# Performance work log

Hardware: AMD Instinct MI355X
Metric: run time of the kernel (lower is better)

## Reference

```python
import jax, jax.numpy as jnp
import numpy as np

N_NODES = 59392        # batch_size * node_each_graph = 512 * 116
N_EDGES = 1187840      # avg degree 20

def _graph_conv(h, src, dst, W, b, out_norm, in_norm):
    # DGL GraphConv, norm='both': act((D_in^-1/2 A D_out^-1/2 h) W + b)
    h = h * out_norm[:, None]
    m = jax.ops.segment_sum(h[src], dst, num_segments=N_NODES)  # sparse aggregation
    m = m * in_norm[:, None]
    return jax.nn.relu(m @ W + b)

def setup_inputs() -> dict:
    key = jax.random.key(0)
    ks = jax.random.split(key, 8)
    feat = jax.random.normal(ks[0], (N_NODES, 116), dtype=jnp.float32)
    src = jax.random.randint(ks[1], (N_EDGES,), 0, N_NODES)
    dst = jax.random.randint(ks[2], (N_EDGES,), 0, N_NODES)
    W1 = jax.random.normal(ks[3], (116, 64), dtype=jnp.float32) * 0.05
    b1 = jnp.zeros((64,), dtype=jnp.float32)
    W2 = jax.random.normal(ks[4], (64, 64), dtype=jnp.float32) * 0.05
    b2 = jnp.zeros((64,), dtype=jnp.float32)
    Wc = jax.random.normal(ks[5], (116 * 64, 2), dtype=jnp.float32) * 0.05
    bc = jnp.zeros((2,), dtype=jnp.float32)
    return {"feat": feat, "src": src, "dst": dst, "batch_size": 512,
            "W1": W1, "b1": b1, "W2": W2, "b2": b2, "Wc": Wc, "bc": bc}

def reference(feat, src, dst, batch_size, W1, b1, W2, b2, Wc, bc):
    ones = jnp.ones((N_EDGES,), dtype=jnp.float32)
    out_deg = jax.ops.segment_sum(ones, src, num_segments=N_NODES)
    in_deg = jax.ops.segment_sum(ones, dst, num_segments=N_NODES)
    out_norm = jax.lax.rsqrt(jnp.maximum(out_deg, 1.0))
    in_norm = jax.lax.rsqrt(jnp.maximum(in_deg, 1.0))
    h = _graph_conv(feat, src, dst, W1, b1, out_norm, in_norm)
    # dropout is identity in eval mode
    h = _graph_conv(h, src, dst, W2, b2, out_norm, in_norm)
    h = h.reshape(batch_size, -1)  # (B, node_each_graph * hid)
    return h @ Wc + bc
```

## Files before the change

### kernel.cpp

```cpp
#include <hip/hip_runtime.h>

#define N_NODES 59392
#define N_EDGES 1187840
#define F_IN 116
#define F_HID 64
#define BATCH 512
#define NPG 116
#define CCAP 64
#define NSLD 160
#define EPSD (N_EDGES / NSLD)
#define NSLS 64
#define EPSS (N_EDGES / NSLS)
#define NR 4
#define NPR4 (N_NODES / NR)
#define GPB 4
#define NPB (NPG / GPB)
#define SCAN_BLK (N_NODES / 256)
#define GEMM_BLK 640

typedef __attribute__((ext_vector_type(8))) short short8;
typedef __attribute__((ext_vector_type(4))) float float4v;

__device__ __forceinline__ float u2f(unsigned u) {
    union { unsigned u; float f; } x; x.u = u; return x.f;
}
__device__ __forceinline__ float bf2f(unsigned short h) {
    union { unsigned u; float f; } x; x.u = (unsigned)h << 16; return x.f;
}
__device__ __forceinline__ unsigned short f2bf(float f) {
    union { float f; unsigned u; } x; x.f = f;
    unsigned r = x.u + 0x7FFF + ((x.u >> 16) & 1);
    return (unsigned short)(r >> 16);
}

__global__ __launch_bounds__(256) void hist_kernel(const int* __restrict__ src,
                                                   const int* __restrict__ dst,
                                                   unsigned short* __restrict__ cnt2,
                                                   unsigned short* __restrict__ cnt2s) {
    __shared__ unsigned bins[NPR4 / 2];
    int tid = threadIdx.x;
    int b = blockIdx.x;
    const int* __restrict__ idx;
    unsigned short* outp;
    int slice, range, nedge;
    if (b < NSLD * NR) {
        slice = b >> 2; range = b & 3; idx = dst; outp = cnt2; nedge = EPSD;
    } else {
        int bb = b - NSLD * NR;
        slice = bb >> 2; range = bb & 3; idx = src; outp = cnt2s; nedge = EPSS;
    }
    int r0 = range * NPR4;
    long ebase = (long)slice * nedge;
    for (int k = tid; k < NPR4 / 2; k += 256) bins[k] = 0;
    __syncthreads();
    for (int k = tid; k < nedge; k += 256) {
        int v = idx[ebase + k] - r0;
        if ((unsigned)v < NPR4) atomicAdd(&bins[v >> 1], 1u << ((v & 1) * 16));
    }
    __syncthreads();
    unsigned* op = (unsigned*)(outp + (size_t)slice * N_NODES + r0);
    for (int k = tid; k < NPR4 / 2; k += 256) op[k] = bins[k];
}

__global__ __launch_bounds__(256) void scan_gemm1_kernel(unsigned short* __restrict__ cnt2,
                                                         const unsigned short* __restrict__ cnt2s,
                                                         float* __restrict__ onorm,
                                                         float* __restrict__ inorm,
                                                         int* __restrict__ ncnt,
                                                         const float* __restrict__ feat,
                                                         const float* __restrict__ W1,
                                                         unsigned short* __restrict__ A1h) {
    if (blockIdx.x < SCAN_BLK) {
        int d = blockIdx.x * 256 + threadIdx.x;
        int run = 0;
        #pragma unroll 1
        for (int i = 0; i < NSLD; i += 8) {
            int c[8];
            #pragma unroll
            for (int j = 0; j < 8; ++j) c[j] = cnt2[(size_t)(i + j) * N_NODES + d];
            #pragma unroll
            for (int j = 0; j < 8; ++j) {
                cnt2[(size_t)(i + j) * N_NODES + d] = (unsigned short)run;
                run += c[j];
            }
        }
        int o = 0;
        #pragma unroll 1
        for (int i = 0; i < NSLS; i += 8) {
            int c[8];
            #pragma unroll
            for (int j = 0; j < 8; ++j) c[j] = cnt2s[(size_t)(i + j) * N_NODES + d];
            #pragma unroll
            for (int j = 0; j < 8; ++j) o += c[j];
        }
        onorm[d] = rsqrtf(fmaxf((float)o, 1.0f));
        inorm[d] = rsqrtf(fmaxf((float)run, 1.0f));
        ncnt[d] = run < CCAP ? run : CCAP;
        if (d == 0) onorm[N_NODES] = 0.f;
        return;
    }
    int lane = threadIdx.x & 63;
    int c16 = lane & 15, quad = lane >> 4;
    short8 Bhi[4][4], Blo[4][4];
    #pragma unroll
    for (int kiter = 0; kiter < 4; ++kiter) {
        #pragma unroll
        for (int t = 0; t < 4; ++t) {
            #pragma unroll
            for (int j = 0; j < 8; ++j) {
                int k = kiter * 32 + quad * 8 + j;
                float w = (k < F_IN) ? W1[k * F_HID + t * 16 + c16] : 0.f;
                unsigned short hi = f2bf(w);
                unsigned short lo = f2bf(w - bf2f(hi));
                Bhi[kiter][t][j] = (short)hi;
                Blo[kiter][t][j] = (short)lo;
            }
        }
    }
    int bid = blockIdx.x - SCAN_BLK;
    int wid = (bid * 256 + threadIdx.x) >> 6;
    int nwaves = (GEMM_BLK * 256) >> 6;
    const int ntiles = N_NODES / 16;
    for (int tile = wid; tile < ntiles; tile += nwaves) {
        int base = tile * 16;
        int row = base + c16;
        const float* fp = feat + (size_t)row * F_IN;
        float4v acc[4] = {{0.f,0.f,0.f,0.f},{0.f,0.f,0.f,0.f},{0.f,0.f,0.f,0.f},{0.f,0.f,0.f,0.f}};
        #pragma unroll
        for (int kiter = 0; kiter < 4; ++kiter) {
            int koff = kiter * 32 + quad * 8;
            float f[8];
            if (koff + 8 <= F_IN) {
                float4 x = *(const float4*)(fp + koff);
                float4 y = *(const float4*)(fp + koff + 4);
                f[0]=x.x; f[1]=x.y; f[2]=x.z; f[3]=x.w;
                f[4]=y.x; f[5]=y.y; f[6]=y.z; f[7]=y.w;
            } else {
                #pragma unroll
                for (int j = 0; j < 8; ++j) f[j] = (koff + j < F_IN) ? fp[koff + j] : 0.f;
            }
            short8 ah, al;
            #pragma unroll
            for (int j = 0; j < 8; ++j) {
                float v = f[j];
                unsigned short hi = f2bf(v);
                ah[j] = (short)hi;
                al[j] = (short)f2bf(v - bf2f(hi));
            }
            #pragma unroll
            for (int t = 0; t < 4; ++t) {
                acc[t] = __builtin_amdgcn_mfma_f32_16x16x32_bf16(ah, Bhi[kiter][t], acc[t], 0, 0, 0);
                acc[t] = __builtin_amdgcn_mfma_f32_16x16x32_bf16(al, Bhi[kiter][t], acc[t], 0, 0, 0);
                acc[t] = __builtin_amdgcn_mfma_f32_16x16x32_bf16(ah, Blo[kiter][t], acc[t], 0, 0, 0);
            }
        }
        #pragma unroll
        for (int t = 0; t < 4; ++t) {
            #pragma unroll
            for (int r = 0; r < 4; ++r) {
                int node = base + quad * 4 + r;
                A1h[(size_t)node * F_HID + t * 16 + c16] = f2bf(acc[t][r]);
            }
        }
    }
}

__global__ __launch_bounds__(256) void place_kernel(const int* __restrict__ src,
                                                    const int* __restrict__ dst,
                                                    const unsigned short* __restrict__ cnt2,
                                                    unsigned short* __restrict__ ebuf) {
    __shared__ unsigned cur[NPR4 / 2];
    int tid = threadIdx.x;
    int slice = blockIdx.x >> 2;
    int r0 = (blockIdx.x & 3) * NPR4;
    long ebase = (long)slice * EPSD;
    const unsigned* pp = (const unsigned*)(cnt2 + (size_t)slice * N_NODES + r0);
    for (int k = tid; k < NPR4 / 2; k += 256) cur[k] = pp[k];
    __syncthreads();
    #pragma unroll 1
    for (int t = 0; t < 7; ++t) {
        int k = t * 1024 + tid;
        int d0 = dst[ebase + k],        s0 = src[ebase + k];
        int d1 = dst[ebase + k + 256],  s1 = src[ebase + k + 256];
        int d2 = dst[ebase + k + 512],  s2 = src[ebase + k + 512];
        int d3 = dst[ebase + k + 768],  s3 = src[ebase + k + 768];
        #define PLACE1(dd, ss)                                                    \
            { int dr = (dd) - r0;                                                 \
              if ((unsigned)dr < NPR4) {                                          \
                  int sh = (dr & 1) * 16;                                         \
                  unsigned old = atomicAdd(&cur[dr >> 1], 1u << sh);              \
                  unsigned pos = (old >> sh) & 0xFFFFu;                           \
                  if (pos < CCAP) ebuf[(size_t)(dd) * CCAP + pos] = (unsigned short)(ss); } }
        PLACE1(d0, s0) PLACE1(d1, s1) PLACE1(d2, s2) PLACE1(d3, s3)
    }
    {
        int k = 7168 + tid;
        int d0 = dst[ebase + k], s0 = src[ebase + k];
        PLACE1(d0, s0)
        #undef PLACE1
    }
}

template<bool ON>
__device__ __forceinline__ void gather2n(const unsigned* __restrict__ base,
                                         const unsigned short* __restrict__ ebuf,
                                         const float* __restrict__ onorm,
                                         int va, int vb, int na, int nb,
                                         int c16, int g4, int sh16,
                                         float& a0, float& a1, float& a2, float& a3,
                                         float& b0, float& b1, float& b2, float& b3) {
    const unsigned long long* ea = (const unsigned long long*)(ebuf + (size_t)va * CCAP);
    const unsigned long long* eb = (const unsigned long long*)(ebuf + (size_t)vb * CCAP);
    unsigned long long cha[8], chb[8];
    #pragma unroll
    for (int t = 0; t < 8; ++t) cha[t] = __builtin_nontemporal_load(&ea[t]);
    #pragma unroll
    for (int t = 0; t < 8; ++t) chb[t] = __builtin_nontemporal_load(&eb[t]);
    int ida[8], idb[8];
    #pragma unroll
    for (int t = 0; t < 8; ++t) {
        ida[t] = (t * 4 + g4 < na) ? (int)((cha[t] >> sh16) & 0xFFFFu) : N_NODES;
        idb[t] = (t * 4 + g4 < nb) ? (int)((chb[t] >> sh16) & 0xFFFFu) : N_NODES;
    }
    unsigned long long rwa[8], rwb[8];
    #pragma unroll
    for (int t = 0; t < 8; ++t) rwa[t] = *(const unsigned long long*)(base + ida[t] * 32 + c16 * 2);
    #pragma unroll
    for (int t = 0; t < 8; ++t) rwb[t] = *(const unsigned long long*)(base + idb[t] * 32 + c16 * 2);
    float oa[8], ob[8];
    if constexpr (ON) {
        #pragma unroll
        for (int t = 0; t < 8; ++t) { oa[t] = onorm[ida[t]]; ob[t] = onorm[idb[t]]; }
    }
    #pragma unroll
    for (int t = 0; t < 8; ++t) {
        unsigned lo = (unsigned)rwa[t], hi = (unsigned)(rwa[t] >> 32);
        float s = ON ? oa[t] : 1.f;
        a0 += s * u2f(lo << 16); a1 += s * u2f(lo & 0xFFFF0000u);
        a2 += s * u2f(hi << 16); a3 += s * u2f(hi & 0xFFFF0000u);
    }
    #pragma unroll
    for (int t = 0; t < 8; ++t) {
        unsigned lo = (unsigned)rwb[t], hi = (unsigned)(rwb[t] >> 32);
        float s = ON ? ob[t] : 1.f;
        b0 += s * u2f(lo << 16); b1 += s * u2f(lo & 0xFFFF0000u);
        b2 += s * u2f(hi << 16); b3 += s * u2f(hi & 0xFFFF0000u);
    }
    int nqa = (na + 3) >> 2;
    #pragma unroll 1
    for (int t = 8; t < nqa; ++t) {
        unsigned long long c = __builtin_nontemporal_load(&ea[t]);
        int e = t * 4 + g4;
        int ix = (e < na) ? (int)((c >> sh16) & 0xFFFFu) : N_NODES;
        unsigned long long w = *(const unsigned long long*)(base + ix * 32 + c16 * 2);
        unsigned lo = (unsigned)w, hi = (unsigned)(w >> 32);
        float s = 1.f;
        if constexpr (ON) s = onorm[ix];
        a0 += s * u2f(lo << 16); a1 += s * u2f(lo & 0xFFFF0000u);
        a2 += s * u2f(hi << 16); a3 += s * u2f(hi & 0xFFFF0000u);
    }
    int nqb = (nb + 3) >> 2;
    #pragma unroll 1
    for (int t = 8; t < nqb; ++t) {
        unsigned long long c = __builtin_nontemporal_load(&eb[t]);
        int e = t * 4 + g4;
        int ix = (e < nb) ? (int)((c >> sh16) & 0xFFFFu) : N_NODES;
        unsigned long long w = *(const unsigned long long*)(base + ix * 32 + c16 * 2);
        unsigned lo = (unsigned)w, hi = (unsigned)(w >> 32);
        float s = 1.f;
        if constexpr (ON) s = onorm[ix];
        b0 += s * u2f(lo << 16); b1 += s * u2f(lo & 0xFFFF0000u);
        b2 += s * u2f(hi << 16); b3 += s * u2f(hi & 0xFFFF0000u);
    }
    a0 += __shfl_xor(a0, 16); a1 += __shfl_xor(a1, 16);
    a2 += __shfl_xor(a2, 16); a3 += __shfl_xor(a3, 16);
    a0 += __shfl_xor(a0, 32); a1 += __shfl_xor(a1, 32);
    a2 += __shfl_xor(a2, 32); a3 += __shfl_xor(a3, 32);
    b0 += __shfl_xor(b0, 16); b1 += __shfl_xor(b1, 16);
    b2 += __shfl_xor(b2, 16); b3 += __shfl_xor(b3, 16);
    b0 += __shfl_xor(b0, 32); b1 += __shfl_xor(b1, 32);
    b2 += __shfl_xor(b2, 32); b3 += __shfl_xor(b3, 32);
}

__global__ __launch_bounds__(256) void gather1_kernel(const int* __restrict__ ncnt,
                                                      const unsigned short* __restrict__ ebuf,
                                                      const unsigned short* __restrict__ A1h,
                                                      const float* __restrict__ onorm,
                                                      const float* __restrict__ inorm,
                                                      const float* __restrict__ b1,
                                                      unsigned short* __restrict__ H1h,
                                                      float* __restrict__ out) {
    if (blockIdx.x == 0) {
        int t = threadIdx.x;
        for (int k = t; k < BATCH * 2; k += 256) out[k] = 0.f;
        if (t < 16) ((unsigned long long*)(H1h + (size_t)N_NODES * F_HID))[t] = 0ull;
    }
    int lane = threadIdx.x & 63;
    int wu = __builtin_amdgcn_readfirstlane(threadIdx.x >> 6);
    int c16 = lane & 15, g4 = lane >> 4, sh16 = g4 * 16;
    int va = blockIdx.x * 8 + wu * 2;
    int vb = va + 1;
    int na = ncnt[va], nb = ncnt[vb];
    const unsigned* base = (const unsigned*)A1h;
    float4 b1q = ((const float4*)b1)[c16];
    float a0 = 0.f, a1 = 0.f, a2 = 0.f, a3 = 0.f;
    float b0 = 0.f, b1v = 0.f, b2v = 0.f, b3 = 0.f;
    gather2n<true>(base, ebuf, onorm, va, vb, na, nb, c16, g4, sh16,
                   a0, a1, a2, a3, b0, b1v, b2v, b3);
    float ina = inorm[va], ona = onorm[va];
    float inb = inorm[vb], onb = onorm[vb];
    float ha0 = fmaxf(ina * a0 + b1q.x, 0.f) * ona;
    float ha1 = fmaxf(ina * a1 + b1q.y, 0.f) * ona;
    float ha2 = fmaxf(ina * a2 + b1q.z, 0.f) * ona;
    float ha3 = fmaxf(ina * a3 + b1q.w, 0.f) * ona;
    float hb0 = fmaxf(inb * b0 + b1q.x, 0.f) * onb;
    float hb1 = fmaxf(inb * b1v + b1q.y, 0.f) * onb;
    float hb2 = fmaxf(inb * b2v + b1q.z, 0.f) * onb;
    float hb3 = fmaxf(inb * b3 + b1q.w, 0.f) * onb;
    if (g4 == 0) {
        unsigned lo = (unsigned)f2bf(ha0) | ((unsigned)f2bf(ha1) << 16);
        unsigned hi = (unsigned)f2bf(ha2) | ((unsigned)f2bf(ha3) << 16);
        ((unsigned long long*)H1h)[(size_t)va * 16 + c16] = ((unsigned long long)hi << 32) | lo;
        lo = (unsigned)f2bf(hb0) | ((unsigned)f2bf(hb1) << 16);
        hi = (unsigned)f2bf(hb2) | ((unsigned)f2bf(hb3) << 16);
        ((unsigned long long*)H1h)[(size_t)vb * 16 + c16] = ((unsigned long long)hi << 32) | lo;
    }
}

__global__ __launch_bounds__(256) void readout_kernel(const int* __restrict__ ncnt,
                                                      const unsigned short* __restrict__ ebuf,
                                                      const unsigned short* __restrict__ H1h,
                                                      const float* __restrict__ inorm,
                                                      const float* __restrict__ b2,
                                                      const float* __restrict__ W2,
                                                      const float* __restrict__ Wc,
                                                      const float* __restrict__ bc,
                                                      float* __restrict__ out) {
    __shared__ float Gs[NPB][F_HID];
    __shared__ float ls[8];
    int g = blockIdx.x >> 2, part = blockIdx.x & 3;
    int nbase = g * NPG + part * NPB;
    int lane = threadIdx.x & 63;
    int wu = __builtin_amdgcn_readfirstlane(threadIdx.x >> 6);
    int c16 = lane & 15, g4 = lane >> 4, sh16 = g4 * 16;
    const unsigned* base = (const unsigned*)H1h;
    for (int nl = wu * 2; nl + 1 < NPB; nl += 8) {
        int va = nbase + nl, vb = va + 1;
        int na = ncnt[va], nb = ncnt[vb];
        float a0 = 0.f, a1 = 0.f, a2 = 0.f, a3 = 0.f;
        float b0 = 0.f, b1 = 0.f, b2v = 0.f, b3 = 0.f;
        gather2n<false>(base, ebuf, (const float*)nullptr, va, vb, na, nb, c16, g4, sh16,
                        a0, a1, a2, a3, b0, b1, b2v, b3);
        if (g4 == 0) {
            float4 m4; m4.x = a0; m4.y = a1; m4.z = a2; m4.w = a3;
            *(float4*)&Gs[nl][c16 * 4] = m4;
            m4.x = b0; m4.y = b1; m4.z = b2v; m4.w = b3;
            *(float4*)&Gs[nl + 1][c16 * 4] = m4;
        }
    }
    if (wu == 2) {
        int v = nbase + 28;
        int n = ncnt[v];
        float a0 = 0.f, a1 = 0.f, a2 = 0.f, a3 = 0.f;
        float d0 = 0.f, d1 = 0.f, d2 = 0.f, d3 = 0.f;
        gather2n<false>(base, ebuf, (const float*)nullptr, v, v, n, 0, c16, g4, sh16,
                        a0, a1, a2, a3, d0, d1, d2, d3);
        if (g4 == 0) {
            float4 m4; m4.x = a0; m4.y = a1; m4.z = a2; m4.w = a3;
            *(float4*)&Gs[28][c16 * 4] = m4;
        }
    }
    __syncthreads();
    float w2[F_HID];
    #pragma unroll
    for (int k = 0; k < F_HID; ++k) w2[k] = W2[k * F_HID + lane];
    float b2l = b2[lane];
    float s0 = 0.f, s1 = 0.f;
    for (int nl = wu; nl < NPB; nl += 4) {
        int v = nbase + nl;
        float acc = 0.f;
        #pragma unroll
        for (int k = 0; k < F_HID; k += 4) {
            float4 gk = *(const float4*)&Gs[nl][k];
            acc += gk.x * w2[k] + gk.y * w2[k + 1] + gk.z * w2[k + 2] + gk.w * w2[k + 3];
        }
        float h = fmaxf(inorm[v] * acc + b2l, 0.f);
        float2 w = ((const float2*)Wc)[(part * NPB + nl) * F_HID + lane];
        s0 += h * w.x;
        s1 += h * w.y;
    }
    #pragma unroll
    for (int off = 32; off > 0; off >>= 1) {
        s0 += __shfl_down(s0, off);
        s1 += __shfl_down(s1, off);
    }
    if (lane == 0) { ls[wu * 2] = s0; ls[wu * 2 + 1] = s1; }
    __syncthreads();
    if (threadIdx.x < 2) {
        float t = 0.f;
        #pragma unroll
        for (int w = 0; w < 4; ++w) t += ls[w * 2 + threadIdx.x];
        if (part == 0) t += bc[threadIdx.x];
        atomicAdd(&out[g * 2 + threadIdx.x], t);
    }
}

extern "C" void kernel_launch(void* const* d_in, const int* in_sizes, int n_in,
                              void* d_out, int out_size, void* d_ws, size_t ws_size,
                              hipStream_t stream) {
    const float* feat = (const float*)d_in[0];
    const int*   src  = (const int*)d_in[1];
    const int*   dst  = (const int*)d_in[2];
    const float* W1 = (const float*)d_in[4];
    const float* b1 = (const float*)d_in[5];
    const float* W2 = (const float*)d_in[6];
    const float* b2 = (const float*)d_in[7];
    const float* Wc = (const float*)d_in[8];
    const float* bc = (const float*)d_in[9];
    float* out = (float*)d_out;

    unsigned short* cnt2  = (unsigned short*)d_ws;
    unsigned short* cnt2s = cnt2 + (size_t)NSLD * N_NODES;
    float* onorm = (float*)(cnt2s + (size_t)NSLS * N_NODES);
    float* inorm = onorm + N_NODES + 1;
    int* ncnt    = (int*)(inorm + N_NODES);
    unsigned short* ebuf = (unsigned short*)(ncnt + N_NODES);
    unsigned short* A1h  = ebuf + (size_t)N_NODES * CCAP;
    unsigned short* H1h  = cnt2;

    hist_kernel<<<NSLD * NR + NSLS * NR, 256, 0, stream>>>(src, dst, cnt2, cnt2s);
    scan_gemm1_kernel<<<SCAN_BLK + GEMM_BLK, 256, 0, stream>>>(cnt2, cnt2s, onorm, inorm,
                                                               ncnt, feat, W1, A1h);
    place_kernel<<<NSLD * NR, 256, 0, stream>>>(src, dst, cnt2, ebuf);
    gather1_kernel<<<N_NODES / 8, 256, 0, stream>>>(ncnt, ebuf, A1h, onorm, inorm, b1, H1h, out);
    readout_kernel<<<BATCH * GPB, 256, 0, stream>>>(ncnt, ebuf, H1h, inorm, b2, W2, Wc, bc, out);
}
```

Before: 225.0 us.

## Replace sliced histogram/scan/place with global atomic edge bucketing fused into GEMM1

Drops the per-slice LDS histograms, prefix scan and separate placement pass. Edges are now bucketed by destination with global atomics on degree counters, in blocks that run alongside the first-layer MFMA GEMM blocks. A small zero kernel runs first. Degree norms are recomputed on the fly with rsqrt instead of being stored, which removes several kernels and the large count arrays. The cost is heavy global atomic contention, and neighbour order within each bucket is now nondeterministic, so float summation order can vary between runs.

```diff
diff --git a/kernel.cpp b/kernel.cpp
--- a/kernel.cpp
+++ b/kernel.cpp
@@ -7,19 +7,15 @@
 #define BATCH 512
 #define NPG 116
 #define CCAP 64
-#define NSLD 160
-#define EPSD (N_EDGES / NSLD)
-#define NSLS 64
-#define EPSS (N_EDGES / NSLS)
-#define NR 4
-#define NPR4 (N_NODES / NR)
 #define GPB 4
 #define NPB (NPG / GPB)
-#define SCAN_BLK (N_NODES / 256)
 #define GEMM_BLK 640
+#define BUILD_BLK 512
+#define ZERO_BLK 64
 
 typedef __attribute__((ext_vector_type(8))) short short8;
 typedef __attribute__((ext_vector_type(4))) float float4v;
+typedef __attribute__((ext_vector_type(4))) int int4v;
 
 __device__ __forceinline__ float u2f(unsigned u) {
     union { unsigned u; float f; } x; x.u = u; return x.f;
@@ -33,70 +29,54 @@
     return (unsigned short)(r >> 16);
 }
 
-__global__ __launch_bounds__(256) void hist_kernel(const int* __restrict__ src,
-                                                   const int* __restrict__ dst,
-                                                   unsigned short* __restrict__ cnt2,
-                                                   unsigned short* __restrict__ cnt2s) {
-    __shared__ unsigned bins[NPR4 / 2];
-    int tid = threadIdx.x;
-    int b = blockIdx.x;
-    const int* __restrict__ idx;
-    unsigned short* outp;
-    int slice, range, nedge;
-    if (b < NSLD * NR) {
-        slice = b >> 2; range = b & 3; idx = dst; outp = cnt2; nedge = EPSD;
-    } else {
-        int bb = b - NSLD * NR;
-        slice = bb >> 2; range = bb & 3; idx = src; outp = cnt2s; nedge = EPSS;
-    }
-    int r0 = range * NPR4;
-    long ebase = (long)slice * nedge;
-    for (int k = tid; k < NPR4 / 2; k += 256) bins[k] = 0;
-    __syncthreads();
-    for (int k = tid; k < nedge; k += 256) {
-        int v = idx[ebase + k] - r0;
-        if ((unsigned)v < NPR4) atomicAdd(&bins[v >> 1], 1u << ((v & 1) * 16));
-    }
-    __syncthreads();
-    unsigned* op = (unsigned*)(outp + (size_t)slice * N_NODES + r0);
-    for (int k = tid; k < NPR4 / 2; k += 256) op[k] = bins[k];
-}
-
-__global__ __launch_bounds__(256) void scan_gemm1_kernel(unsigned short* __restrict__ cnt2,
-                                                         const unsigned short* __restrict__ cnt2s,
-                                                         float* __restrict__ onorm,
-                                                         float* __restrict__ inorm,
-                                                         int* __restrict__ ncnt,
-                                                         const float* __restrict__ feat,
-                                                         const float* __restrict__ W1,
-                                                         unsigned short* __restrict__ A1h) {
-    if (blockIdx.x < SCAN_BLK) {
-        int d = blockIdx.x * 256 + threadIdx.x;
-        int run = 0;
+__global__ __launch_bounds__(256) void zero_kernel(unsigned* __restrict__ odeg,
+                                                   unsigned* __restrict__ icnt,
+                                                   unsigned short* __restrict__ A1h,
+                                                   unsigned short* __restrict__ H1h,
+                                                   float* __restrict__ out) {
+    int gid = blockIdx.x * 256 + threadIdx.x;
+    for (int k = gid; k < N_NODES + 1; k += ZERO_BLK * 256) {
+        odeg[k] = 0u;
+        icnt[k] = 0u;
+    }
+    if (blockIdx.x == 0) {
+        if (threadIdx.x < 16) {
+            ((unsigned long long*)(A1h + (size_t)N_NODES * F_HID))[threadIdx.x] = 0ull;
+            ((unsigned long long*)(H1h + (size_t)N_NODES * F_HID))[threadIdx.x] = 0ull;
+        }
+        for (int k = threadIdx.x; k < BATCH * 2; k += 256) out[k] = 0.f;
+    }
+}
+
+__global__ __launch_bounds__(256) void build_gemm1_kernel(const int* __restrict__ src,
+                                                          const int* __restrict__ dst,
+                                                          unsigned* __restrict__ odeg,
+                                                          unsigned* __restrict__ icnt,
+                                                          unsigned short* __restrict__ ebuf,
+                                                          const float* __restrict__ feat,
+                                                          const float* __restrict__ W1,
+                                                          unsigned short* __restrict__ A1h) {
+    if (blockIdx.x >= GEMM_BLK) {
+        int gid = (blockIdx.x - GEMM_BLK) * 256 + threadIdx.x;
+        const int4v* s4 = (const int4v*)src;
+        const int4v* d4 = (const int4v*)dst;
         #pragma unroll 1
-        for (int i = 0; i < NSLD; i += 8) {
-            int c[8];
-            #pragma unroll
-            for (int j = 0; j < 8; ++j) c[j] = cnt2[(size_t)(i + j) * N_NODES + d];
-            #pragma unroll
-            for (int j = 0; j < 8; ++j) {
-                cnt2[(size_t)(i + j) * N_NODES + d] = (unsigned short)run;
-                run += c[j];
-            }
-        }
-        int o = 0;
-        #pragma unroll 1
-        for (int i = 0; i < NSLS; i += 8) {
-            int c[8];
-            #pragma unroll
-            for (int j = 0; j < 8; ++j) c[j] = cnt2s[(size_t)(i + j) * N_NODES + d];
-            #pragma unroll
-            for (int j = 0; j < 8; ++j) o += c[j];
-        }
-        onorm[d] = rsqrtf(fmaxf((float)o, 1.0f));
-        inorm[d] = rsqrtf(fmaxf((float)run, 1.0f));
-        ncnt[d] = run < CCAP ? run : CCAP;
-        if (d == 0) onorm[N_NODES] = 0.f;
+        for (int k = gid; k < N_EDGES / 4; k += BUILD_BLK * 256) {
+            int4v s = __builtin_nontemporal_load(&s4[k]);
+            int4v d = __builtin_nontemporal_load(&d4[k]);
+            atomicAdd(&odeg[s.x], 1u);
+            atomicAdd(&odeg[s.y], 1u);
+            atomicAdd(&odeg[s.z], 1u);
+            atomicAdd(&odeg[s.w], 1u);
+            unsigned p0 = atomicAdd(&icnt[d.x], 1u);
+            unsigned p1 = atomicAdd(&icnt[d.y], 1u);
+            unsigned p2 = atomicAdd(&icnt[d.z], 1u);
+            unsigned p3 = atomicAdd(&icnt[d.w], 1u);
+            if (p0 < CCAP) ebuf[(size_t)d.x * CCAP + p0] = (unsigned short)s.x;
+            if (p1 < CCAP) ebuf[(size_t)d.y * CCAP + p1] = (unsigned short)s.y;
+            if (p2 < CCAP) ebuf[(size_t)d.z * CCAP + p2] = (unsigned short)s.z;
+            if (p3 < CCAP) ebuf[(size_t)d.w * CCAP + p3] = (unsigned short)s.w;
+        }
         return;
     }
     int lane = threadIdx.x & 63;
@@ -117,8 +97,7 @@
             }
         }
     }
-    int bid = blockIdx.x - SCAN_BLK;
-    int wid = (bid * 256 + threadIdx.x) >> 6;
+    int wid = (blockIdx.x * 256 + threadIdx.x) >> 6;
     int nwaves = (GEMM_BLK * 256) >> 6;
     const int ntiles = N_NODES / 16;
     for (int tile = wid; tile < ntiles; tile += nwaves) {
@@ -165,46 +144,10 @@
     }
 }
 
-__global__ __launch_bounds__(256) void place_kernel(const int* __restrict__ src,
-                                                    const int* __restrict__ dst,
-                                                    const unsigned short* __restrict__ cnt2,
-                                                    unsigned short* __restrict__ ebuf) {
-    __shared__ unsigned cur[NPR4 / 2];
-    int tid = threadIdx.x;
-    int slice = blockIdx.x >> 2;
-    int r0 = (blockIdx.x & 3) * NPR4;
-    long ebase = (long)slice * EPSD;
-    const unsigned* pp = (const unsigned*)(cnt2 + (size_t)slice * N_NODES + r0);
-    for (int k = tid; k < NPR4 / 2; k += 256) cur[k] = pp[k];
-    __syncthreads();
-    #pragma unroll 1
-    for (int t = 0; t < 7; ++t) {
-        int k = t * 1024 + tid;
-        int d0 = dst[ebase + k],        s0 = src[ebase + k];
-        int d1 = dst[ebase + k + 256],  s1 = src[ebase + k + 256];
-        int d2 = dst[ebase + k + 512],  s2 = src[ebase + k + 512];
-        int d3 = dst[ebase + k + 768],  s3 = src[ebase + k + 768];
-        #define PLACE1(dd, ss)                                                    \
-            { int dr = (dd) - r0;                                                 \
-              if ((unsigned)dr < NPR4) {                                          \
-                  int sh = (dr & 1) * 16;                                         \
-                  unsigned old = atomicAdd(&cur[dr >> 1], 1u << sh);              \
-                  unsigned pos = (old >> sh) & 0xFFFFu;                           \
-                  if (pos < CCAP) ebuf[(size_t)(dd) * CCAP + pos] = (unsigned short)(ss); } }
-        PLACE1(d0, s0) PLACE1(d1, s1) PLACE1(d2, s2) PLACE1(d3, s3)
-    }
-    {
-        int k = 7168 + tid;
-        int d0 = dst[ebase + k], s0 = src[ebase + k];
-        PLACE1(d0, s0)
-        #undef PLACE1
-    }
-}
-
 template<bool ON>
 __device__ __forceinline__ void gather2n(const unsigned* __restrict__ base,
                                          const unsigned short* __restrict__ ebuf,
-                                         const float* __restrict__ onorm,
+                                         const unsigned* __restrict__ odeg,
                                          int va, int vb, int na, int nb,
                                          int c16, int g4, int sh16,
                                          float& a0, float& a1, float& a2, float& a3,
@@ -229,8 +172,14 @@
     for (int t = 0; t < 8; ++t) rwb[t] = *(const unsigned long long*)(base + idb[t] * 32 + c16 * 2);
     float oa[8], ob[8];
     if constexpr (ON) {
-        #pragma unroll
-        for (int t = 0; t < 8; ++t) { oa[t] = onorm[ida[t]]; ob[t] = onorm[idb[t]]; }
+        unsigned dga[8], dgb[8];
+        #pragma unroll
+        for (int t = 0; t < 8; ++t) { dga[t] = odeg[ida[t]]; dgb[t] = odeg[idb[t]]; }
+        #pragma unroll
+        for (int t = 0; t < 8; ++t) {
+            oa[t] = rsqrtf(fmaxf((float)dga[t], 1.f));
+            ob[t] = rsqrtf(fmaxf((float)dgb[t], 1.f));
+        }
     }
     #pragma unroll
     for (int t = 0; t < 8; ++t) {
@@ -255,7 +204,7 @@
         unsigned long long w = *(const unsigned long long*)(base + ix * 32 + c16 * 2);
         unsigned lo = (unsigned)w, hi = (unsigned)(w >> 32);
         float s = 1.f;
-        if constexpr (ON) s = onorm[ix];
+        if constexpr (ON) s = rsqrtf(fmaxf((float)odeg[ix], 1.f));
         a0 += s * u2f(lo << 16); a1 += s * u2f(lo & 0xFFFF0000u);
         a2 += s * u2f(hi << 16); a3 += s * u2f(hi & 0xFFFF0000u);
     }
@@ -268,7 +217,7 @@
         unsigned long long w = *(const unsigned long long*)(base + ix * 32 + c16 * 2);
         unsigned lo = (unsigned)w, hi = (unsigned)(w >> 32);
         float s = 1.f;
-        if constexpr (ON) s = onorm[ix];
+        if constexpr (ON) s = rsqrtf(fmaxf((float)odeg[ix], 1.f));
         b0 += s * u2f(lo << 16); b1 += s * u2f(lo & 0xFFFF0000u);
         b2 += s * u2f(hi << 16); b3 += s * u2f(hi & 0xFFFF0000u);
     }
@@ -282,33 +231,30 @@
     b2 += __shfl_xor(b2, 32); b3 += __shfl_xor(b3, 32);
 }
 
-__global__ __launch_bounds__(256) void gather1_kernel(const int* __restrict__ ncnt,
+__global__ __launch_bounds__(256) void gather1_kernel(const unsigned* __restrict__ odeg,
+                                                      const unsigned* __restrict__ icnt,
                                                       const unsigned short* __restrict__ ebuf,
                                                       const unsigned short* __restrict__ A1h,
-                                                      const float* __restrict__ onorm,
-                                                      const float* __restrict__ inorm,
                                                       const float* __restrict__ b1,
-                                                      unsigned short* __restrict__ H1h,
-                                                      float* __restrict__ out) {
-    if (blockIdx.x == 0) {
-        int t = threadIdx.x;
-        for (int k = t; k < BATCH * 2; k += 256) out[k] = 0.f;
-        if (t < 16) ((unsigned long long*)(H1h + (size_t)N_NODES * F_HID))[t] = 0ull;
-    }
+                                                      unsigned short* __restrict__ H1h) {
     int lane = threadIdx.x & 63;
     int wu = __builtin_amdgcn_readfirstlane(threadIdx.x >> 6);
     int c16 = lane & 15, g4 = lane >> 4, sh16 = g4 * 16;
     int va = blockIdx.x * 8 + wu * 2;
     int vb = va + 1;
-    int na = ncnt[va], nb = ncnt[vb];
+    unsigned ca = icnt[va], cb = icnt[vb];
+    int na = ca < CCAP ? (int)ca : CCAP;
+    int nb = cb < CCAP ? (int)cb : CCAP;
     const unsigned* base = (const unsigned*)A1h;
     float4 b1q = ((const float4*)b1)[c16];
     float a0 = 0.f, a1 = 0.f, a2 = 0.f, a3 = 0.f;
     float b0 = 0.f, b1v = 0.f, b2v = 0.f, b3 = 0.f;
-    gather2n<true>(base, ebuf, onorm, va, vb, na, nb, c16, g4, sh16,
+    gather2n<true>(base, ebuf, odeg, va, vb, na, nb, c16, g4, sh16,
                    a0, a1, a2, a3, b0, b1v, b2v, b3);
-    float ina = inorm[va], ona = onorm[va];
-    float inb = inorm[vb], onb = onorm[vb];
+    float ina = rsqrtf(fmaxf((float)ca, 1.f));
+    float inb = rsqrtf(fmaxf((float)cb, 1.f));
+    float ona = rsqrtf(fmaxf((float)odeg[va], 1.f));
+    float onb = rsqrtf(fmaxf((float)odeg[vb], 1.f));
     float ha0 = fmaxf(ina * a0 + b1q.x, 0.f) * ona;
     float ha1 = fmaxf(ina * a1 + b1q.y, 0.f) * ona;
     float ha2 = fmaxf(ina * a2 + b1q.z, 0.f) * ona;
@@ -327,10 +273,9 @@
     }
 }
 
-__global__ __launch_bounds__(256) void readout_kernel(const int* __restrict__ ncnt,
+__global__ __launch_bounds__(256) void readout_kernel(const unsigned* __restrict__ icnt,
                                                       const unsigned short* __restrict__ ebuf,
                                                       const unsigned short* __restrict__ H1h,
-                                                      const float* __restrict__ inorm,
                                                       const float* __restrict__ b2,
                                                       const float* __restrict__ W2,
                                                       const float* __restrict__ Wc,
@@ -346,10 +291,12 @@
     const unsigned* base = (const unsigned*)H1h;
     for (int nl = wu * 2; nl + 1 < NPB; nl += 8) {
         int va = nbase + nl, vb = va + 1;
-        int na = ncnt[va], nb = ncnt[vb];
+        unsigned ta = icnt[va], tb = icnt[vb];
+        int na = ta < CCAP ? (int)ta : CCAP;
+        int nb = tb < CCAP ? (int)tb : CCAP;
         float a0 = 0.f, a1 = 0.f, a2 = 0.f, a3 = 0.f;
         float b0 = 0.f, b1 = 0.f, b2v = 0.f, b3 = 0.f;
-        gather2n<false>(base, ebuf, (const float*)nullptr, va, vb, na, nb, c16, g4, sh16,
+        gather2n<false>(base, ebuf, (const unsigned*)nullptr, va, vb, na, nb, c16, g4, sh16,
                         a0, a1, a2, a3, b0, b1, b2v, b3);
         if (g4 == 0) {
             float4 m4; m4.x = a0; m4.y = a1; m4.z = a2; m4.w = a3;
@@ -360,10 +307,11 @@
     }
     if (wu == 2) {
         int v = nbase + 28;
-        int n = ncnt[v];
+        unsigned tv = icnt[v];
+        int n = tv < CCAP ? (int)tv : CCAP;
         float a0 = 0.f, a1 = 0.f, a2 = 0.f, a3 = 0.f;
         float d0 = 0.f, d1 = 0.f, d2 = 0.f, d3 = 0.f;
-        gather2n<false>(base, ebuf, (const float*)nullptr, v, v, n, 0, c16, g4, sh16,
+        gather2n<false>(base, ebuf, (const unsigned*)nullptr, v, v, n, 0, c16, g4, sh16,
                         a0, a1, a2, a3, d0, d1, d2, d3);
         if (g4 == 0) {
             float4 m4; m4.x = a0; m4.y = a1; m4.z = a2; m4.w = a3;
@@ -384,7 +332,8 @@
             float4 gk = *(const float4*)&Gs[nl][k];
             acc += gk.x * w2[k] + gk.y * w2[k + 1] + gk.z * w2[k + 2] + gk.w * w2[k + 3];
         }
-        float h = fmaxf(inorm[v] * acc + b2l, 0.f);
+        float inv = rsqrtf(fmaxf((float)icnt[v], 1.f));
+        float h = fmaxf(inv * acc + b2l, 0.f);
         float2 w = ((const float2*)Wc)[(part * NPB + nl) * F_HID + lane];
         s0 += h * w.x;
         s1 += h * w.y;
@@ -419,19 +368,15 @@
     const float* bc = (const float*)d_in[9];
     float* out = (float*)d_out;
 
-    unsigned short* cnt2  = (unsigned short*)d_ws;
-    unsigned short* cnt2s = cnt2 + (size_t)NSLD * N_NODES;
-    float* onorm = (float*)(cnt2s + (size_t)NSLS * N_NODES);
-    float* inorm = onorm + N_NODES + 1;
-    int* ncnt    = (int*)(inorm + N_NODES);
-    unsigned short* ebuf = (unsigned short*)(ncnt + N_NODES);
+    unsigned* odeg = (unsigned*)d_ws;
+    unsigned* icnt = odeg + (N_NODES + 1);
+    unsigned short* ebuf = (unsigned short*)(icnt + (N_NODES + 1));
     unsigned short* A1h  = ebuf + (size_t)N_NODES * CCAP;
-    unsigned short* H1h  = cnt2;
-
-    hist_kernel<<<NSLD * NR + NSLS * NR, 256, 0, stream>>>(src, dst, cnt2, cnt2s);
-    scan_gemm1_kernel<<<SCAN_BLK + GEMM_BLK, 256, 0, stream>>>(cnt2, cnt2s, onorm, inorm,
-                                                               ncnt, feat, W1, A1h);
-    place_kernel<<<NSLD * NR, 256, 0, stream>>>(src, dst, cnt2, ebuf);
-    gather1_kernel<<<N_NODES / 8, 256, 0, stream>>>(ncnt, ebuf, A1h, onorm, inorm, b1, H1h, out);
-    readout_kernel<<<BATCH * GPB, 256, 0, stream>>>(ncnt, ebuf, H1h, inorm, b2, W2, Wc, bc, out);
-}
+    unsigned short* H1h  = A1h + (size_t)(N_NODES + 1) * F_HID;
+
+    zero_kernel<<<ZERO_BLK, 256, 0, stream>>>(odeg, icnt, A1h, H1h, out);
+    build_gemm1_kernel<<<GEMM_BLK + BUILD_BLK, 256, 0, stream>>>(src, dst, odeg, icnt, ebuf,
+                                                                 feat, W1, A1h);
+    gather1_kernel<<<N_NODES / 8, 256, 0, stream>>>(odeg, icnt, ebuf, A1h, b1, H1h);
+    readout_kernel<<<BATCH * GPB, 256, 0, stream>>>(icnt, ebuf, H1h, b2, W2, Wc, bc, out);
+}
```

New measurement: 273.9 us. +21.8%, slower.

## Use full-node LDS histograms with 1024-thread blocks in hist and place kernels

Applied to the files above, without the earlier changes.

The histogram and placement kernels now keep one shared-memory bin array covering all nodes (about 116 KB of LDS) and run one 1024-thread block per edge slice. Before, each slice was split into four node ranges, so every block re-read the whole slice and discarded three quarters of it. This removes those redundant edge reads and the range filtering, at the cost of fewer blocks with high LDS use, which limits occupancy to one block per CU. It also reduces the source-histogram slice count, aligns ebuf to 256 bytes, and zeroes a padding row of A1h.

```diff
diff --git a/kernel.cpp b/kernel.cpp
--- a/kernel.cpp
+++ b/kernel.cpp
@@ -9,10 +9,9 @@
 #define CCAP 64
 #define NSLD 160
 #define EPSD (N_EDGES / NSLD)
-#define NSLS 64
+#define NSLS 40
 #define EPSS (N_EDGES / NSLS)
-#define NR 4
-#define NPR4 (N_NODES / NR)
+#define NBIN (N_NODES / 2)
 #define GPB 4
 #define NPB (NPG / GPB)
 #define SCAN_BLK (N_NODES / 256)
@@ -33,33 +32,31 @@
     return (unsigned short)(r >> 16);
 }
 
-__global__ __launch_bounds__(256) void hist_kernel(const int* __restrict__ src,
-                                                   const int* __restrict__ dst,
-                                                   unsigned short* __restrict__ cnt2,
-                                                   unsigned short* __restrict__ cnt2s) {
-    __shared__ unsigned bins[NPR4 / 2];
+__global__ __launch_bounds__(1024) void hist_kernel(const int* __restrict__ src,
+                                                    const int* __restrict__ dst,
+                                                    unsigned short* __restrict__ cnt2,
+                                                    unsigned short* __restrict__ cnt2s) {
+    __shared__ unsigned bins[NBIN];
     int tid = threadIdx.x;
     int b = blockIdx.x;
     const int* __restrict__ idx;
     unsigned short* outp;
-    int slice, range, nedge;
-    if (b < NSLD * NR) {
-        slice = b >> 2; range = b & 3; idx = dst; outp = cnt2; nedge = EPSD;
+    int slice, nedge;
+    if (b < NSLD) {
+        slice = b; idx = dst; outp = cnt2; nedge = EPSD;
     } else {
-        int bb = b - NSLD * NR;
-        slice = bb >> 2; range = bb & 3; idx = src; outp = cnt2s; nedge = EPSS;
-    }
-    int r0 = range * NPR4;
+        slice = b - NSLD; idx = src; outp = cnt2s; nedge = EPSS;
+    }
     long ebase = (long)slice * nedge;
-    for (int k = tid; k < NPR4 / 2; k += 256) bins[k] = 0;
+    for (int k = tid; k < NBIN; k += 1024) bins[k] = 0;
     __syncthreads();
-    for (int k = tid; k < nedge; k += 256) {
-        int v = idx[ebase + k] - r0;
-        if ((unsigned)v < NPR4) atomicAdd(&bins[v >> 1], 1u << ((v & 1) * 16));
+    for (int k = tid; k < nedge; k += 1024) {
+        int v = idx[ebase + k];
+        atomicAdd(&bins[v >> 1], 1u << ((v & 1) * 16));
     }
     __syncthreads();
-    unsigned* op = (unsigned*)(outp + (size_t)slice * N_NODES + r0);
-    for (int k = tid; k < NPR4 / 2; k += 256) op[k] = bins[k];
+    unsigned* op = (unsigned*)(outp + (size_t)slice * N_NODES);
+    for (int k = tid; k < NBIN; k += 1024) op[k] = bins[k];
 }
 
 __global__ __launch_bounds__(256) void scan_gemm1_kernel(unsigned short* __restrict__ cnt2,
@@ -97,6 +94,8 @@
         inorm[d] = rsqrtf(fmaxf((float)run, 1.0f));
         ncnt[d] = run < CCAP ? run : CCAP;
         if (d == 0) onorm[N_NODES] = 0.f;
+        if (blockIdx.x == 0 && threadIdx.x < 16)
+            ((unsigned long long*)(A1h + (size_t)N_NODES * F_HID))[threadIdx.x] = 0ull;
         return;
     }
     int lane = threadIdx.x & 63;
@@ -165,39 +164,24 @@
     }
 }
 
-__global__ __launch_bounds__(256) void place_kernel(const int* __restrict__ src,
-                                                    const int* __restrict__ dst,
-                                                    const unsigned short* __restrict__ cnt2,
-                                                    unsigned short* __restrict__ ebuf) {
-    __shared__ unsigned cur[NPR4 / 2];
+__global__ __launch_bounds__(1024) void place_kernel(const int* __restrict__ src,
+                                                     const int* __restrict__ dst,
+                                                     const unsigned short* __restrict__ cnt2,
+                                                     unsigned short* __restrict__ ebuf) {
+    __shared__ unsigned cur[NBIN];
     int tid = threadIdx.x;
-    int slice = blockIdx.x >> 2;
-    int r0 = (blockIdx.x & 3) * NPR4;
+    int slice = blockIdx.x;
     long ebase = (long)slice * EPSD;
-    const unsigned* pp = (const unsigned*)(cnt2 + (size_t)slice * N_NODES + r0);
-    for (int k = tid; k < NPR4 / 2; k += 256) cur[k] = pp[k];
+    const unsigned* pp = (const unsigned*)(cnt2 + (size_t)slice * N_NODES);
+    for (int k = tid; k < NBIN; k += 1024) cur[k] = pp[k];
     __syncthreads();
     #pragma unroll 1
-    for (int t = 0; t < 7; ++t) {
-        int k = t * 1024 + tid;
-        int d0 = dst[ebase + k],        s0 = src[ebase + k];
-        int d1 = dst[ebase + k + 256],  s1 = src[ebase + k + 256];
-        int d2 = dst[ebase + k + 512],  s2 = src[ebase + k + 512];
-        int d3 = dst[ebase + k + 768],  s3 = src[ebase + k + 768];
-        #define PLACE1(dd, ss)                                                    \
-            { int dr = (dd) - r0;                                                 \
-              if ((unsigned)dr < NPR4) {                                          \
-                  int sh = (dr & 1) * 16;                                         \
-                  unsigned old = atomicAdd(&cur[dr >> 1], 1u << sh);              \
-                  unsigned pos = (old >> sh) & 0xFFFFu;                           \
-                  if (pos < CCAP) ebuf[(size_t)(dd) * CCAP + pos] = (unsigned short)(ss); } }
-        PLACE1(d0, s0) PLACE1(d1, s1) PLACE1(d2, s2) PLACE1(d3, s3)
-    }
-    {
-        int k = 7168 + tid;
-        int d0 = dst[ebase + k], s0 = src[ebase + k];
-        PLACE1(d0, s0)
-        #undef PLACE1
+    for (int k = tid; k < EPSD; k += 1024) {
+        int d = dst[ebase + k], s = src[ebase + k];
+        int sh = (d & 1) * 16;
+        unsigned old = atomicAdd(&cur[d >> 1], 1u << sh);
+        unsigned pos = (old >> sh) & 0xFFFFu;
+        if (pos < CCAP) ebuf[(size_t)d * CCAP + pos] = (unsigned short)s;
     }
 }
 
@@ -424,14 +408,14 @@
     float* onorm = (float*)(cnt2s + (size_t)NSLS * N_NODES);
     float* inorm = onorm + N_NODES + 1;
     int* ncnt    = (int*)(inorm + N_NODES);
-    unsigned short* ebuf = (unsigned short*)(ncnt + N_NODES);
+    unsigned short* ebuf = (unsigned short*)(((unsigned long long)(ncnt + N_NODES) + 255ull) & ~255ull);
     unsigned short* A1h  = ebuf + (size_t)N_NODES * CCAP;
     unsigned short* H1h  = cnt2;
 
-    hist_kernel<<<NSLD * NR + NSLS * NR, 256, 0, stream>>>(src, dst, cnt2, cnt2s);
+    hist_kernel<<<NSLD + NSLS, 1024, 0, stream>>>(src, dst, cnt2, cnt2s);
     scan_gemm1_kernel<<<SCAN_BLK + GEMM_BLK, 256, 0, stream>>>(cnt2, cnt2s, onorm, inorm,
                                                                ncnt, feat, W1, A1h);
-    place_kernel<<<NSLD * NR, 256, 0, stream>>>(src, dst, cnt2, ebuf);
+    place_kernel<<<NSLD, 1024, 0, stream>>>(src, dst, cnt2, ebuf);
     gather1_kernel<<<N_NODES / 8, 256, 0, stream>>>(ncnt, ebuf, A1h, onorm, inorm, b1, H1h, out);
     readout_kernel<<<BATCH * GPB, 256, 0, stream>>>(ncnt, ebuf, H1h, inorm, b2, W2, Wc, bc, out);
 }
```

Result: faster. 205.9 us (-8.5%).
